# Kernel optimization log

Hardware: AMD Instinct MI355X
Metric: run time of the kernel (lower is better)

The kernel has to match this reference:

```python
import jax, jax.numpy as jnp
import numpy as np

CONF = 0.25      # args.conf
IOU_THR = 0.45   # args.iou
MAX_DET = 300    # args.max_det
NC = 80          # len(model.names)
CAND = 2048      # static cap: top-scoring candidates entering NMS (jit-friendly stand-in for boolean conf mask)


def setup_inputs():
    key = jax.random.key(0)
    pred = jax.random.uniform(key, (16, 4 + NC, 8400), dtype=jnp.float32)
    # first 4 channels are xywh in pixel coordinates for a 640x640 image
    pred = pred.at[:, :4, :].multiply(640.0)
    return {"pred": pred, "img_size": 640}


def xywh2xyxy(b):
    xy, wh = b[..., :2], b[..., 2:4]
    return jnp.concatenate([xy - wh * 0.5, xy + wh * 0.5], axis=-1)


def box_iou(b):
    # b: (K, 4) xyxy -> (K, K) pairwise IoU (torchvision convention)
    x1, y1, x2, y2 = b[:, 0], b[:, 1], b[:, 2], b[:, 3]
    area = (x2 - x1) * (y2 - y1)
    ix1 = jnp.maximum(x1[:, None], x1[None, :])
    iy1 = jnp.maximum(y1[:, None], y1[None, :])
    ix2 = jnp.minimum(x2[:, None], x2[None, :])
    iy2 = jnp.minimum(y2[:, None], y2[None, :])
    inter = jnp.clip(ix2 - ix1, 0.0) * jnp.clip(iy2 - iy1, 0.0)
    return inter / (area[:, None] + area[None, :] - inter + 1e-7)


def nms_keep(nmsbox, valid):
    # Greedy NMS over boxes already sorted by descending score.
    iou = box_iou(nmsbox)  # (CAND, CAND)

    def body(keep, i):
        suppressed = jnp.any(keep & (iou[i] > IOU_THR))
        ki = valid[i] & jnp.logical_not(suppressed)
        return keep.at[i].set(ki), None

    keep0 = jnp.zeros((nmsbox.shape[0],), dtype=bool)
    keep, _ = jax.lax.scan(body, keep0, jnp.arange(nmsbox.shape[0]))
    return keep


def _forward(pred, img_size):
    p = jnp.transpose(pred, (0, 2, 1))           # (N, A, 4+NC)
    boxes_xywh = p[..., :4]
    cls_scores = p[..., 4:4 + NC]
    scores = jnp.max(cls_scores, axis=-1)        # (N, A)
    classes = jnp.argmax(cls_scores, axis=-1)    # (N, A) int

    # static top-CAND candidates (score > conf handled via valid mask below)
    top_s, top_i = jax.lax.top_k(scores, CAND)   # sorted descending
    box = jnp.take_along_axis(boxes_xywh, top_i[..., None], axis=1)  # (N, CAND, 4)
    cls = jnp.take_along_axis(classes, top_i, axis=1)                # (N, CAND)
    box = xywh2xyxy(box)
    inv = 1.0 / img_size                          # multiplier=1, divide by max(H, W)

    def per_image(box_i, score_i, cls_i):
        valid = score_i > CONF
        # class-aware NMS: add class id offset to all 4 normalized coords
        nmsbox = box_i * inv + cls_i[:, None].astype(box_i.dtype)
        keep = nms_keep(nmsbox, valid)
        # kept boxes first, in score order; rest pushed to the end and zeroed
        order = jnp.argsort(jnp.where(keep, jnp.arange(CAND), CAND))[:MAX_DET]
        kept = keep[order].astype(box_i.dtype)[:, None]
        dets = jnp.concatenate(
            [box_i[order], score_i[order, None], cls_i[order, None].astype(box_i.dtype)],
            axis=-1,
        )  # (MAX_DET, 6)
        return dets * kept

    return jax.vmap(per_image)(box, top_s, cls)   # (N, MAX_DET, 6)


def reference(pred, img_size):
    return _forward(pred, img_size)
```

## Files before the change

### kernel.cpp

```cpp
#include <hip/hip_runtime.h>
#include <stdint.h>

#define NB 16
#define NA 8400
#define NA_PAD 9216
#define NCH 84
#define NCLS 80
#define CANDN 2048
#define MAXDET 300

typedef unsigned long long u64;

static const size_t OFF_SU   = 0;
static const size_t OFF_CLS  = 537600;
static const size_t OFF_BOX  = 1075200;
static const size_t OFF_KEY  = 3225600;
static const size_t OFF_NMSB = 3487744;
static const size_t OFF_AREA = 4012032;
static const size_t OFF_H12  = 4143104;
static const size_t OFF_H16  = 4405248;
static const size_t OFF_CLSB = 8599552;

__global__ __launch_bounds__(256) void zero_kernel(int* __restrict__ h) {
  h[blockIdx.x * 256 + threadIdx.x] = 0;
}

__global__ __launch_bounds__(256) void score_kernel(const float* __restrict__ pred,
                                                    unsigned* __restrict__ sug,
                                                    int* __restrict__ cls,
                                                    float4* __restrict__ boxT,
                                                    int* __restrict__ h12,
                                                    int* __restrict__ h16) {
  int a = blockIdx.x * 256 + threadIdx.x;
  int b = blockIdx.y;
  if (a >= NA) return;
  int lane = threadIdx.x & 63;
  const float* pbase = pred + (size_t)b * (NCH * NA);
  const float* p = pbase + 4 * NA + a;
  float best = p[0];
  int bc = 0;
#pragma unroll 8
  for (int c = 1; c < NCLS; ++c) {
    float v = p[(size_t)c * NA];
    if (v > best) { best = v; bc = c; }
  }
  unsigned u = ~__float_as_uint(best);
  sug[(size_t)b * NA + a] = u;
  cls[(size_t)b * NA + a] = bc;
  boxT[(size_t)b * NA + a] =
      make_float4(pbase[a], pbase[NA + a], pbase[2 * NA + a], pbase[3 * NA + a]);
  u64 m = __ballot(true);
  u64 m12 = 0;
#pragma unroll
  for (int bit = 31; bit >= 16; --bit) {
    u64 bb = __ballot((u >> bit) & 1);
    m &= ((u >> bit) & 1) ? bb : ~bb;
    if (bit == 20) m12 = m;
  }
  u64 below = (lane == 0) ? 0ULL : ((1ULL << lane) - 1ULL);
  if ((m12 & below) == 0ULL)
    atomicAdd(&h12[b * 4096 + (int)(u >> 20)], (int)__popcll(m12));
  if ((m & below) == 0ULL)
    atomicAdd(&h16[b * 65536 + (int)(u >> 16)], (int)__popcll(m));
}

__device__ inline u64 shflx64(u64 v, int m) {
  int lo = __shfl_xor((int)(unsigned)(v & 0xFFFFFFFFu), m, 64);
  int hi = __shfl_xor((int)(unsigned)(v >> 32), m, 64);
  return (((u64)(unsigned)hi) << 32) | (unsigned)lo;
}

__device__ inline u64 cswap(u64 a, u64 b, int s, int j, int kk) {
  bool low = (s & j) == 0;
  bool asc = (s & kk) == 0;
  bool takeMin = (low == asc);
  u64 mn = (a < b) ? a : b;
  u64 mx = (a < b) ? b : a;
  return takeMin ? mn : mx;
}

__device__ inline bool iou_gt(float4 bi, float ai, float4 bj, float aj) {
  const double THR = 0x1.CCCCCC8p-2;
  float ix1 = fmaxf(bi.x, bj.x);
  float iy1 = fmaxf(bi.y, bj.y);
  float ix2 = fminf(bi.z, bj.z);
  float iy2 = fminf(bi.w, bj.w);
  float iw = fmaxf(__fsub_rn(ix2, ix1), 0.0f);
  float ih = fmaxf(__fsub_rn(iy2, iy1), 0.0f);
  float inter = __fmul_rn(iw, ih);
  float den = __fadd_rn(__fsub_rn(__fadd_rn(ai, aj), inter), 1e-7f);
  return (double)inter > THR * (double)den;
}

__global__ __launch_bounds__(1024) void select_kernel(const unsigned* __restrict__ sug,
                                                      const int* __restrict__ h12g,
                                                      const int* __restrict__ h16g,
                                                      u64* __restrict__ keybuf) {
  __shared__ alignas(16) unsigned su[NA];
  __shared__ int hist8[256];
  __shared__ int cum[256];
  __shared__ int tielist[1024];
  __shared__ int sl16[16];
  __shared__ int wtot[16];
  __shared__ unsigned sh_pref;
  __shared__ int sh_k, sh_g, sh_cnt;

  int b = blockIdx.x;
  int tid = threadIdx.x;
  int lane = tid & 63;
  int wv = tid >> 6;

  if (tid == 0) { sh_pref = 0; sh_k = CANDN; sh_g = 0; sh_cnt = 0; }

  {
    uint4* su4 = (uint4*)su;
    const uint4* sg4 = (const uint4*)(sug + (size_t)b * NA);
    for (int v = tid; v < NA / 4; v += 1024) su4[v] = sg4[v];
  }

  const int* hb = h12g + b * 4096;
  int4 v = ((const int4*)hb)[tid];
  int ssum = v.x + v.y + v.z + v.w;
  int incl = ssum;
  for (int off = 1; off < 64; off <<= 1) {
    int t = __shfl_up(incl, off, 64);
    if (lane >= off) incl += t;
  }
  if (lane == 63) wtot[wv] = incl;
  __syncthreads();
  if (tid < 16) {
    int w0 = wtot[tid];
    int inc2 = w0;
    for (int off = 1; off < 16; off <<= 1) {
      int t = __shfl_up(inc2, off, 16);
      if (tid >= off) inc2 += t;
    }
    wtot[tid] = inc2 - w0;
  }
  __syncthreads();
  int ebase = wtot[wv] + incl - ssum;
  if (ebase < CANDN && ebase + ssum >= CANDN) {
    int c = ebase;
    int hh[4] = {v.x, v.y, v.z, v.w};
#pragma unroll
    for (int t = 0; t < 4; ++t) {
      if (c + hh[t] >= CANDN) { sh_pref = (unsigned)(tid * 4 + t); sh_k = CANDN - c; break; }
      c += hh[t];
    }
  }
  __syncthreads();
  unsigned B12 = sh_pref;
  int k = sh_k;

  if (tid < 16) sl16[tid] = h16g[(size_t)b * 65536 + B12 * 16 + tid];
  __syncthreads();
  if (tid == 0) {
    int c = 0;
#pragma unroll
    for (int j = 0; j < 16; ++j) {
      int h = sl16[j];
      if (c + h >= k) { sh_pref = (B12 << 4) + (unsigned)j; sh_k = k - c; break; }
      c += h;
    }
  }
  __syncthreads();
  unsigned B16 = sh_pref;
  k = sh_k;

  if (tid < 256) hist8[tid] = 0;
  __syncthreads();
  for (int i = tid; i < NA; i += 1024) {
    unsigned u = su[i];
    if ((u >> 16) == B16) atomicAdd(&hist8[(u >> 8) & 255], 1);
  }
  __syncthreads();
  if (tid < 64) {
    int v0 = hist8[tid * 4 + 0], v1 = hist8[tid * 4 + 1];
    int v2 = hist8[tid * 4 + 2], v3 = hist8[tid * 4 + 3];
    int s0 = v0, s1 = s0 + v1, s2 = s1 + v2, s3 = s2 + v3;
    int tot = s3;
    for (int off = 1; off < 64; off <<= 1) {
      int t = __shfl_up(tot, off, 64);
      if (tid >= off) tot += t;
    }
    int base = tot - s3;
    cum[tid * 4 + 0] = base + s0;
    cum[tid * 4 + 1] = base + s1;
    cum[tid * 4 + 2] = base + s2;
    cum[tid * 4 + 3] = base + s3;
  }
  __syncthreads();
  if (tid < 256) {
    int c = cum[tid];
    int cprev = (tid == 0) ? 0 : cum[tid - 1];
    if (c >= k && cprev < k) {
      sh_pref = (B16 << 16) | ((unsigned)tid << 8);
      sh_k = k - cprev;
    }
  }
  __syncthreads();
  unsigned p24 = sh_pref;
  k = sh_k;

  if (tid < 256) hist8[tid] = 0;
  __syncthreads();
  for (int i = tid; i < NA; i += 1024) {
    unsigned u = su[i];
    if ((u & 0xFFFFFF00u) == p24) atomicAdd(&hist8[u & 255], 1);
  }
  __syncthreads();
  if (tid < 64) {
    int v0 = hist8[tid * 4 + 0], v1 = hist8[tid * 4 + 1];
    int v2 = hist8[tid * 4 + 2], v3 = hist8[tid * 4 + 3];
    int s0 = v0, s1 = s0 + v1, s2 = s1 + v2, s3 = s2 + v3;
    int tot = s3;
    for (int off = 1; off < 64; off <<= 1) {
      int t = __shfl_up(tot, off, 64);
      if (tid >= off) tot += t;
    }
    int base = tot - s3;
    cum[tid * 4 + 0] = base + s0;
    cum[tid * 4 + 1] = base + s1;
    cum[tid * 4 + 2] = base + s2;
    cum[tid * 4 + 3] = base + s3;
  }
  __syncthreads();
  if (tid < 256) {
    int c = cum[tid];
    int cprev = (tid == 0) ? 0 : cum[tid - 1];
    if (c >= k && cprev < k) {
      sh_pref = p24 | (unsigned)tid;
      sh_k = k - cprev;
    }
  }
  __syncthreads();
  unsigned ustar = sh_pref;
  int kp = sh_k;

  for (int i = tid; i < NA; i += 1024) {
    if (su[i] == ustar) {
      int p = atomicAdd(&sh_g, 1);
      if (p < 1024) tielist[p] = i;
    }
  }
  __syncthreads();
  int g = sh_g < 1024 ? sh_g : 1024;

  for (int i = tid; i < NA_PAD; i += 1024) {
    bool act = false;
    u64 key = 0;
    if (i < NA) {
      unsigned u = su[i];
      if (u < ustar) act = true;
      else if (u == ustar) {
        int r = 0;
        for (int t2 = 0; t2 < g; ++t2) r += (tielist[t2] < i);
        act = (r < kp);
      }
      key = (((u64)u) << 32) | (unsigned)i;
    }
    u64 mm = __ballot(act);
    if (mm) {
      int leader = __ffsll(mm) - 1;
      int base = 0;
      if (lane == leader) base = atomicAdd(&sh_cnt, (int)__popcll(mm));
      base = __shfl(base, leader, 64);
      if (act)
        keybuf[(size_t)b * CANDN + base + (int)__popcll(mm & ((1ULL << lane) - 1))] = key;
    }
  }
}

__global__ __launch_bounds__(256) void prep_kernel(const u64* __restrict__ keybuf,
                                                   const int* __restrict__ clsg,
                                                   const float4* __restrict__ boxTg,
                                                   const int* __restrict__ imgsz,
                                                   float4* __restrict__ nmsbG,
                                                   float* __restrict__ areaG,
                                                   unsigned char* __restrict__ clsbG) {
  int s = blockIdx.x * 256 + threadIdx.x;
  int b = blockIdx.y;
  int o = b * CANDN + s;
  u64 key = keybuf[o];
  int idx = (int)(unsigned)(key & 0xFFFFFFFFu);
  float4 bx = boxTg[(size_t)b * NA + idx];
  float inv = (float)(1.0 / (double)imgsz[0]);
  float hw = __fmul_rn(bx.z, 0.5f);
  float hh = __fmul_rn(bx.w, 0.5f);
  float x1 = __fsub_rn(bx.x, hw);
  float y1 = __fsub_rn(bx.y, hh);
  float x2 = __fadd_rn(bx.x, hw);
  float y2 = __fadd_rn(bx.y, hh);
  int ci = clsg[(size_t)b * NA + idx];
  float clsf = (float)ci;
  float nx1 = __fadd_rn(__fmul_rn(x1, inv), clsf);
  float ny1 = __fadd_rn(__fmul_rn(y1, inv), clsf);
  float nx2 = __fadd_rn(__fmul_rn(x2, inv), clsf);
  float ny2 = __fadd_rn(__fmul_rn(y2, inv), clsf);
  float ar = __fmul_rn(__fsub_rn(nx2, nx1), __fsub_rn(ny2, ny1));
  nmsbG[o] = make_float4(nx1, ny1, nx2, ny2);
  areaG[o] = ar;
  clsbG[o] = (unsigned char)ci;
}

__global__ __launch_bounds__(1024) void nms_kernel(const u64* __restrict__ keybuf,
                                                   const float4* __restrict__ nmsbG,
                                                   const float* __restrict__ areaG,
                                                   const unsigned char* __restrict__ clsbG,
                                                   const int* __restrict__ clsg,
                                                   const float4* __restrict__ boxTg,
                                                   float* __restrict__ out) {
  __shared__ alignas(16) u64 skey[CANDN];
  __shared__ alignas(16) float4 nmsb[CANDN];
  __shared__ float areaA[CANDN];
  __shared__ unsigned short a2s[NA];
  __shared__ unsigned char clsA[CANDN];
  __shared__ float4 chunkbox[64];
  __shared__ float chunkarea[64];
  __shared__ float4 bbox[NCLS][16];
  __shared__ float barea[NCLS][16];
  __shared__ int bcount[NCLS];
  __shared__ float4 ovfbox[MAXDET];
  __shared__ float ovfarea[MAXDET];
  __shared__ int idxbuf[MAXDET];
  __shared__ u64 diag[64];
  __shared__ u64 supx[4];
  __shared__ u64 vmaskc;
  __shared__ int sh_nms, sh_ovf;

  int b = blockIdx.x;
  int tid = threadIdx.x;
  int lane = tid & 63;
  int wv = tid >> 6;

  if (tid == 0) { sh_nms = 0; sh_ovf = 0; }
  if (tid < NCLS) bcount[tid] = 0;

  for (int s = tid; s < CANDN; s += 1024) {
    u64 key = keybuf[(size_t)b * CANDN + s];
    skey[s] = key;
    nmsb[s] = nmsbG[(size_t)b * CANDN + s];
    areaA[s] = areaG[(size_t)b * CANDN + s];
    clsA[s] = clsbG[(size_t)b * CANDN + s];
    a2s[(unsigned)(key & 0xFFFFFFFFu)] = (unsigned short)s;
  }
  __syncthreads();

  int s0 = (wv << 7) + lane;
  int s1 = s0 + 64;
  u64 e0 = skey[s0];
  u64 e1 = skey[s1];
  for (int kk = 2; kk <= CANDN; kk <<= 1) {
    for (int j = kk >> 1; j > 0; j >>= 1) {
      if (j >= 128) {
        skey[s0] = e0;
        skey[s1] = e1;
        __syncthreads();
        u64 p0 = skey[s0 ^ j];
        u64 p1 = skey[s1 ^ j];
        e0 = cswap(e0, p0, s0, j, kk);
        e1 = cswap(e1, p1, s1, j, kk);
        __syncthreads();
      } else if (j == 64) {
        bool asc = (s0 & kk) == 0;
        u64 mn = (e0 < e1) ? e0 : e1;
        u64 mx = (e0 < e1) ? e1 : e0;
        e0 = asc ? mn : mx;
        e1 = asc ? mx : mn;
      } else {
        u64 p0 = shflx64(e0, j);
        u64 p1 = shflx64(e1, j);
        e0 = cswap(e0, p0, s0, j, kk);
        e1 = cswap(e1, p1, s1, j, kk);
      }
    }
  }
  skey[s0] = e0;
  skey[s1] = e1;
  __syncthreads();

#pragma unroll 1
  for (int c = 0; c < 32; ++c) {
    __syncthreads();
    int nk0 = sh_nms;
    if (nk0 >= MAXDET) break;
    int rank = (c << 6) + lane;
    u64 mykey = skey[rank];
    int slot = a2s[(unsigned)(mykey & 0xFFFFFFFFu)];
    float4 br = nmsb[slot];
    float arr = areaA[slot];
    int myc = clsA[slot];
    if (wv == 0) {
      chunkbox[lane] = br;
      chunkarea[lane] = arr;
      u64 vb = __ballot(__uint_as_float(~(unsigned)(mykey >> 32)) > 0.25f);
      if (lane == 0) vmaskc = vb;
    }
    if (wv < 3) {
      int cc = myc - 1 + wv;
      bool ok = (cc >= 0 && cc < NCLS);
      int n = ok ? bcount[cc] : 0;
      bool sup = false;
      for (int q = 0; q < n; ++q)
        sup = sup || iou_gt(br, arr, bbox[cc][q], barea[cc][q]);
      u64 sm = __ballot(sup);
      if (lane == 0) supx[wv] = sm;
    } else if (wv == 3) {
      int n = sh_ovf;
      bool sup = false;
      for (int q = 0; q < n; ++q)
        sup = sup || iou_gt(br, arr, ovfbox[q], ovfarea[q]);
      u64 sm = __ballot(sup);
      if (lane == 0) supx[3] = sm;
    }
    __syncthreads();
    u64 tentg = vmaskc & ~(supx[0] | supx[1] | supx[2] | supx[3]);
#pragma unroll
    for (int rr = 0; rr < 4; ++rr) {
      int r = (wv << 2) + rr;
      if ((tentg >> r) & 1ULL) {
        bool supd = iou_gt(chunkbox[r], chunkarea[r], br, arr);
        u64 bb = __ballot(supd);
        if (lane == 0) diag[r] = bb;
      } else if (lane == 0) {
        diag[r] = 0ULL;
      }
    }
    __syncthreads();
    if (wv == 0) {
      bool tent = ((tentg >> lane) & 1ULL) != 0ULL;
      u64 below = (lane == 0) ? 0ULL : ((1ULL << lane) - 1ULL);
      u64 colbelow = diag[lane] & below;
      u64 kept = __ballot(tent);
      for (int it = 0; it < 64; ++it) {
        bool alive = tent && ((kept & colbelow) == 0ULL);
        u64 nk = __ballot(alive);
        if (nk == kept) break;
        kept = nk;
      }
      int cnt = nk0 + (int)__popcll(kept);
      if (cnt > MAXDET) cnt = MAXDET;
      bool mine = ((kept >> lane) & 1ULL) != 0ULL;
      int pos = nk0 + (int)__popcll(kept & below);
      if (mine && pos < MAXDET) {
        idxbuf[pos] = rank;
        int n = atomicAdd(&bcount[myc], 1);
        if (n < 16) { bbox[myc][n] = br; barea[myc][n] = arr; }
        else {
          int mo = atomicAdd(&sh_ovf, 1);
          ovfbox[mo] = br;
          ovfarea[mo] = arr;
        }
      }
      if (lane == 0) sh_nms = cnt;
    }
  }
  __syncthreads();

  int total = sh_nms;
  if (tid < MAXDET) {
    float vals[6] = {0.f, 0.f, 0.f, 0.f, 0.f, 0.f};
    if (tid < total) {
      int rank = idxbuf[tid];
      u64 key = skey[rank];
      int idx = (int)(unsigned)(key & 0xFFFFFFFFu);
      float score = __uint_as_float(~(unsigned)(key >> 32));
      float4 bx = boxTg[(size_t)b * NA + idx];
      float hw = __fmul_rn(bx.z, 0.5f);
      float hh = __fmul_rn(bx.w, 0.5f);
      vals[0] = __fsub_rn(bx.x, hw);
      vals[1] = __fsub_rn(bx.y, hh);
      vals[2] = __fadd_rn(bx.x, hw);
      vals[3] = __fadd_rn(bx.y, hh);
      vals[4] = score;
      vals[5] = (float)clsg[(size_t)b * NA + idx];
    }
#pragma unroll
    for (int q = 0; q < 6; ++q)
      out[((size_t)(b * MAXDET) + tid) * 6 + q] = vals[q];
  }
}

extern "C" void kernel_launch(void* const* d_in, const int* in_sizes, int n_in,
                              void* d_out, int out_size, void* d_ws, size_t ws_size,
                              hipStream_t stream) {
  (void)in_sizes; (void)n_in; (void)out_size; (void)ws_size;
  const float* pred = (const float*)d_in[0];
  const int* imgsz = (const int*)d_in[1];
  char* ws = (char*)d_ws;
  unsigned* sug = (unsigned*)(ws + OFF_SU);
  int* cls = (int*)(ws + OFF_CLS);
  float4* boxT = (float4*)(ws + OFF_BOX);
  u64* keybuf = (u64*)(ws + OFF_KEY);
  float4* nmsbG = (float4*)(ws + OFF_NMSB);
  float* areaG = (float*)(ws + OFF_AREA);
  int* h12 = (int*)(ws + OFF_H12);
  int* h16 = (int*)(ws + OFF_H16);
  unsigned char* clsb = (unsigned char*)(ws + OFF_CLSB);
  float* out = (float*)d_out;

  zero_kernel<<<(262144 + 4194304) / 4 / 256, 256, 0, stream>>>(h12);
  score_kernel<<<dim3((NA + 255) / 256, NB), 256, 0, stream>>>(pred, sug, cls, boxT,
                                                               h12, h16);
  select_kernel<<<NB, 1024, 0, stream>>>(sug, h12, h16, keybuf);
  prep_kernel<<<dim3(CANDN / 256, NB), 256, 0, stream>>>(keybuf, cls, boxT, imgsz,
                                                         nmsbG, areaG, clsb);
  nms_kernel<<<NB, 1024, 0, stream>>>(keybuf, nmsbG, areaG, clsb, cls, boxT, out);
}
```

Before: 66.81 us.

## Run chunked NMS loop in a single wavefront without block barriers

The greedy NMS chunk loop moves from four cooperating wavefronts that hand off through shared memory and several __syncthreads per chunk to a single wavefront that does all the work. That one wave checks the three neighbouring class buckets and the overflow list, then builds the intra-chunk suppression matrix by iterating only over tentatively-kept rows, prefetching the next row. Barrier overhead and the full diagonal pass disappear, but the single wave now does the per-chunk suppression checks serially, with less parallelism.

```diff
diff --git a/kernel.cpp b/kernel.cpp
--- a/kernel.cpp
+++ b/kernel.cpp
@@ -323,9 +323,6 @@
   __shared__ float4 ovfbox[MAXDET];
   __shared__ float ovfarea[MAXDET];
   __shared__ int idxbuf[MAXDET];
-  __shared__ u64 diag[64];
-  __shared__ u64 supx[4];
-  __shared__ u64 vmaskc;
   __shared__ int sh_nms, sh_ovf;
 
   int b = blockIdx.x;
@@ -379,81 +376,92 @@
   skey[s1] = e1;
   __syncthreads();
 
+  if (wv == 0) {
+    int nk0 = 0;
+    int ovf = 0;
+    u64 below = (lane == 0) ? 0ULL : ((1ULL << lane) - 1ULL);
 #pragma unroll 1
-  for (int c = 0; c < 32; ++c) {
-    __syncthreads();
-    int nk0 = sh_nms;
-    if (nk0 >= MAXDET) break;
-    int rank = (c << 6) + lane;
-    u64 mykey = skey[rank];
-    int slot = a2s[(unsigned)(mykey & 0xFFFFFFFFu)];
-    float4 br = nmsb[slot];
-    float arr = areaA[slot];
-    int myc = clsA[slot];
-    if (wv == 0) {
+    for (int c = 0; c < 32 && nk0 < MAXDET; ++c) {
+      int rank = (c << 6) + lane;
+      u64 mykey = skey[rank];
+      int slot = a2s[(unsigned)(mykey & 0xFFFFFFFFu)];
+      float4 br = nmsb[slot];
+      float arr = areaA[slot];
+      int myc = clsA[slot];
       chunkbox[lane] = br;
       chunkarea[lane] = arr;
-      u64 vb = __ballot(__uint_as_float(~(unsigned)(mykey >> 32)) > 0.25f);
-      if (lane == 0) vmaskc = vb;
-    }
-    if (wv < 3) {
-      int cc = myc - 1 + wv;
-      bool ok = (cc >= 0 && cc < NCLS);
-      int n = ok ? bcount[cc] : 0;
+      bool valid = __uint_as_float(~(unsigned)(mykey >> 32)) > 0.25f;
       bool sup = false;
-      for (int q = 0; q < n; ++q)
-        sup = sup || iou_gt(br, arr, bbox[cc][q], barea[cc][q]);
-      u64 sm = __ballot(sup);
-      if (lane == 0) supx[wv] = sm;
-    } else if (wv == 3) {
-      int n = sh_ovf;
-      bool sup = false;
-      for (int q = 0; q < n; ++q)
+#pragma unroll
+      for (int t = 0; t < 3; ++t) {
+        int cc = myc - 1 + t;
+        if (cc >= 0 && cc < NCLS) {
+          int n = bcount[cc];
+          if (n > 16) n = 16;
+          for (int q = 0; q < n; ++q)
+            sup = sup || iou_gt(br, arr, bbox[cc][q], barea[cc][q]);
+        }
+      }
+      for (int q = 0; q < ovf; ++q)
         sup = sup || iou_gt(br, arr, ovfbox[q], ovfarea[q]);
-      u64 sm = __ballot(sup);
-      if (lane == 0) supx[3] = sm;
-    }
-    __syncthreads();
-    u64 tentg = vmaskc & ~(supx[0] | supx[1] | supx[2] | supx[3]);
-#pragma unroll
-    for (int rr = 0; rr < 4; ++rr) {
-      int r = (wv << 2) + rr;
-      if ((tentg >> r) & 1ULL) {
-        bool supd = iou_gt(chunkbox[r], chunkarea[r], br, arr);
-        u64 bb = __ballot(supd);
-        if (lane == 0) diag[r] = bb;
-      } else if (lane == 0) {
-        diag[r] = 0ULL;
+      bool tent = valid && !sup;
+      u64 tentg = __ballot(tent);
+      if (tentg == 0ULL) continue;
+      u64 colb = 0ULL;
+      {
+        u64 mask = tentg;
+        int i0 = -1;
+        float4 b0 = br;
+        float a0 = arr;
+        if (mask) {
+          i0 = __ffsll(mask) - 1;
+          mask &= mask - 1;
+          b0 = chunkbox[i0];
+          a0 = chunkarea[i0];
+        }
+        while (i0 >= 0) {
+          int i1 = -1;
+          float4 b1 = br;
+          float a1 = arr;
+          if (mask) {
+            i1 = __ffsll(mask) - 1;
+            mask &= mask - 1;
+            b1 = chunkbox[i1];
+            a1 = chunkarea[i1];
+          }
+          u64 bb = __ballot(iou_gt(b0, a0, br, arr));
+          if (lane > i0) colb |= ((bb >> lane) & 1ULL) << i0;
+          i0 = i1;
+          b0 = b1;
+          a0 = a1;
+        }
       }
-    }
-    __syncthreads();
-    if (wv == 0) {
-      bool tent = ((tentg >> lane) & 1ULL) != 0ULL;
-      u64 below = (lane == 0) ? 0ULL : ((1ULL << lane) - 1ULL);
-      u64 colbelow = diag[lane] & below;
-      u64 kept = __ballot(tent);
-      for (int it = 0; it < 64; ++it) {
-        bool alive = tent && ((kept & colbelow) == 0ULL);
+      u64 kept = tentg;
+      while (true) {
+        bool alive = tent && ((kept & colb) == 0ULL);
         u64 nk = __ballot(alive);
         if (nk == kept) break;
         kept = nk;
       }
-      int cnt = nk0 + (int)__popcll(kept);
-      if (cnt > MAXDET) cnt = MAXDET;
       bool mine = ((kept >> lane) & 1ULL) != 0ULL;
       int pos = nk0 + (int)__popcll(kept & below);
       if (mine && pos < MAXDET) {
         idxbuf[pos] = rank;
         int n = atomicAdd(&bcount[myc], 1);
-        if (n < 16) { bbox[myc][n] = br; barea[myc][n] = arr; }
-        else {
+        if (n < 16) {
+          bbox[myc][n] = br;
+          barea[myc][n] = arr;
+        } else {
           int mo = atomicAdd(&sh_ovf, 1);
           ovfbox[mo] = br;
           ovfarea[mo] = arr;
         }
       }
-      if (lane == 0) sh_nms = cnt;
-    }
+      nk0 += (int)__popcll(kept);
+      if (nk0 > MAXDET) nk0 = MAXDET;
+      ovf = sh_ovf;
+    }
+    if (lane == 0) sh_nms = nk0;
   }
   __syncthreads();
 
```

Measured after the change: 110.9 us. 1.66x slower.

## Replace in-block bitonic sort with rank-by-counting scatter in prep kernel

Applied to the files above, without the earlier changes.

The per-image bitonic sort of the 2048 candidate keys inside the single-block NMS kernel is replaced by a counting rank in the prep kernel. Each of 128 blocks computes every key's rank by comparing it against all 2048 keys held in shared memory, then scatters the box, area, class and key directly into sorted order. This removes the barrier-heavy sort and the a2s index indirection from the 16-block NMS kernel, spreading the ordering work across many more blocks at the cost of O(N^2) comparisons. The NMS chunk loop also drops one barrier by folding the valid-mask ballot into wave 0 and computing the diagonal IoU for every row unconditionally.

```diff
diff --git a/kernel.cpp b/kernel.cpp
--- a/kernel.cpp
+++ b/kernel.cpp
@@ -20,6 +20,7 @@
 static const size_t OFF_H12  = 4143104;
 static const size_t OFF_H16  = 4405248;
 static const size_t OFF_CLSB = 8599552;
+static const size_t OFF_KEYR = 8632320;
 
 __global__ __launch_bounds__(256) void zero_kernel(int* __restrict__ h) {
   h[blockIdx.x * 256 + threadIdx.x] = 0;
@@ -64,21 +65,6 @@
     atomicAdd(&h16[b * 65536 + (int)(u >> 16)], (int)__popcll(m));
 }
 
-__device__ inline u64 shflx64(u64 v, int m) {
-  int lo = __shfl_xor((int)(unsigned)(v & 0xFFFFFFFFu), m, 64);
-  int hi = __shfl_xor((int)(unsigned)(v >> 32), m, 64);
-  return (((u64)(unsigned)hi) << 32) | (unsigned)lo;
-}
-
-__device__ inline u64 cswap(u64 a, u64 b, int s, int j, int kk) {
-  bool low = (s & j) == 0;
-  bool asc = (s & kk) == 0;
-  bool takeMin = (low == asc);
-  u64 mn = (a < b) ? a : b;
-  u64 mx = (a < b) ? b : a;
-  return takeMin ? mn : mx;
-}
-
 __device__ inline bool iou_gt(float4 bi, float ai, float4 bj, float aj) {
   const double THR = 0x1.CCCCCC8p-2;
   float ix1 = fmaxf(bi.x, bj.x);
@@ -271,18 +257,25 @@
   }
 }
 
-__global__ __launch_bounds__(256) void prep_kernel(const u64* __restrict__ keybuf,
-                                                   const int* __restrict__ clsg,
-                                                   const float4* __restrict__ boxTg,
-                                                   const int* __restrict__ imgsz,
-                                                   float4* __restrict__ nmsbG,
-                                                   float* __restrict__ areaG,
-                                                   unsigned char* __restrict__ clsbG) {
-  int s = blockIdx.x * 256 + threadIdx.x;
+__global__ __launch_bounds__(256) void rankprep_kernel(const u64* __restrict__ keybuf,
+                                                       const int* __restrict__ clsg,
+                                                       const float4* __restrict__ boxTg,
+                                                       const int* __restrict__ imgsz,
+                                                       u64* __restrict__ skeyR,
+                                                       float4* __restrict__ nmsbR,
+                                                       float* __restrict__ areaR,
+                                                       unsigned char* __restrict__ clsR) {
+  __shared__ alignas(16) u64 kb[CANDN];
   int b = blockIdx.y;
-  int o = b * CANDN + s;
-  u64 key = keybuf[o];
-  int idx = (int)(unsigned)(key & 0xFFFFFFFFu);
+  int tid = threadIdx.x;
+  for (int i = tid; i < CANDN; i += 256) kb[i] = keybuf[(size_t)b * CANDN + i];
+  __syncthreads();
+  int s = blockIdx.x * 256 + tid;
+  u64 mykey = kb[s];
+  int rank = 0;
+#pragma unroll 16
+  for (int j = 0; j < CANDN; ++j) rank += (kb[j] < mykey);
+  int idx = (int)(unsigned)(mykey & 0xFFFFFFFFu);
   float4 bx = boxTg[(size_t)b * NA + idx];
   float inv = (float)(1.0 / (double)imgsz[0]);
   float hw = __fmul_rn(bx.z, 0.5f);
@@ -298,12 +291,14 @@
   float nx2 = __fadd_rn(__fmul_rn(x2, inv), clsf);
   float ny2 = __fadd_rn(__fmul_rn(y2, inv), clsf);
   float ar = __fmul_rn(__fsub_rn(nx2, nx1), __fsub_rn(ny2, ny1));
-  nmsbG[o] = make_float4(nx1, ny1, nx2, ny2);
-  areaG[o] = ar;
-  clsbG[o] = (unsigned char)ci;
-}
-
-__global__ __launch_bounds__(1024) void nms_kernel(const u64* __restrict__ keybuf,
+  int o = b * CANDN + rank;
+  skeyR[o] = mykey;
+  nmsbR[o] = make_float4(nx1, ny1, nx2, ny2);
+  areaR[o] = ar;
+  clsR[o] = (unsigned char)ci;
+}
+
+__global__ __launch_bounds__(1024) void nms_kernel(const u64* __restrict__ skeyRg,
                                                    const float4* __restrict__ nmsbG,
                                                    const float* __restrict__ areaG,
                                                    const unsigned char* __restrict__ clsbG,
@@ -313,10 +308,7 @@
   __shared__ alignas(16) u64 skey[CANDN];
   __shared__ alignas(16) float4 nmsb[CANDN];
   __shared__ float areaA[CANDN];
-  __shared__ unsigned short a2s[NA];
   __shared__ unsigned char clsA[CANDN];
-  __shared__ float4 chunkbox[64];
-  __shared__ float chunkarea[64];
   __shared__ float4 bbox[NCLS][16];
   __shared__ float barea[NCLS][16];
   __shared__ int bcount[NCLS];
@@ -325,7 +317,6 @@
   __shared__ int idxbuf[MAXDET];
   __shared__ u64 diag[64];
   __shared__ u64 supx[4];
-  __shared__ u64 vmaskc;
   __shared__ int sh_nms, sh_ovf;
 
   int b = blockIdx.x;
@@ -337,47 +328,11 @@
   if (tid < NCLS) bcount[tid] = 0;
 
   for (int s = tid; s < CANDN; s += 1024) {
-    u64 key = keybuf[(size_t)b * CANDN + s];
-    skey[s] = key;
+    skey[s] = skeyRg[(size_t)b * CANDN + s];
     nmsb[s] = nmsbG[(size_t)b * CANDN + s];
     areaA[s] = areaG[(size_t)b * CANDN + s];
     clsA[s] = clsbG[(size_t)b * CANDN + s];
-    a2s[(unsigned)(key & 0xFFFFFFFFu)] = (unsigned short)s;
-  }
-  __syncthreads();
-
-  int s0 = (wv << 7) + lane;
-  int s1 = s0 + 64;
-  u64 e0 = skey[s0];
-  u64 e1 = skey[s1];
-  for (int kk = 2; kk <= CANDN; kk <<= 1) {
-    for (int j = kk >> 1; j > 0; j >>= 1) {
-      if (j >= 128) {
-        skey[s0] = e0;
-        skey[s1] = e1;
-        __syncthreads();
-        u64 p0 = skey[s0 ^ j];
-        u64 p1 = skey[s1 ^ j];
-        e0 = cswap(e0, p0, s0, j, kk);
-        e1 = cswap(e1, p1, s1, j, kk);
-        __syncthreads();
-      } else if (j == 64) {
-        bool asc = (s0 & kk) == 0;
-        u64 mn = (e0 < e1) ? e0 : e1;
-        u64 mx = (e0 < e1) ? e1 : e0;
-        e0 = asc ? mn : mx;
-        e1 = asc ? mx : mn;
-      } else {
-        u64 p0 = shflx64(e0, j);
-        u64 p1 = shflx64(e1, j);
-        e0 = cswap(e0, p0, s0, j, kk);
-        e1 = cswap(e1, p1, s1, j, kk);
-      }
-    }
-  }
-  skey[s0] = e0;
-  skey[s1] = e1;
-  __syncthreads();
+  }
 
 #pragma unroll 1
   for (int c = 0; c < 32; ++c) {
@@ -385,21 +340,14 @@
     int nk0 = sh_nms;
     if (nk0 >= MAXDET) break;
     int rank = (c << 6) + lane;
-    u64 mykey = skey[rank];
-    int slot = a2s[(unsigned)(mykey & 0xFFFFFFFFu)];
-    float4 br = nmsb[slot];
-    float arr = areaA[slot];
-    int myc = clsA[slot];
-    if (wv == 0) {
-      chunkbox[lane] = br;
-      chunkarea[lane] = arr;
-      u64 vb = __ballot(__uint_as_float(~(unsigned)(mykey >> 32)) > 0.25f);
-      if (lane == 0) vmaskc = vb;
-    }
+    float4 br = nmsb[rank];
+    float arr = areaA[rank];
+    int myc = clsA[rank];
     if (wv < 3) {
       int cc = myc - 1 + wv;
       bool ok = (cc >= 0 && cc < NCLS);
       int n = ok ? bcount[cc] : 0;
+      if (n > 16) n = 16;
       bool sup = false;
       for (int q = 0; q < n; ++q)
         sup = sup || iou_gt(br, arr, bbox[cc][q], barea[cc][q]);
@@ -413,27 +361,25 @@
       u64 sm = __ballot(sup);
       if (lane == 0) supx[3] = sm;
     }
-    __syncthreads();
-    u64 tentg = vmaskc & ~(supx[0] | supx[1] | supx[2] | supx[3]);
 #pragma unroll
     for (int rr = 0; rr < 4; ++rr) {
       int r = (wv << 2) + rr;
-      if ((tentg >> r) & 1ULL) {
-        bool supd = iou_gt(chunkbox[r], chunkarea[r], br, arr);
-        u64 bb = __ballot(supd);
-        if (lane == 0) diag[r] = bb;
-      } else if (lane == 0) {
-        diag[r] = 0ULL;
-      }
+      bool supd = iou_gt(nmsb[(c << 6) + r], areaA[(c << 6) + r], br, arr);
+      u64 bb = __ballot(supd);
+      if (lane == 0) diag[r] = bb;
     }
     __syncthreads();
     if (wv == 0) {
+      bool valid = __uint_as_float(~(unsigned)(skey[rank] >> 32)) > 0.25f;
+      u64 vb = __ballot(valid);
+      u64 orsup = supx[0] | supx[1] | supx[2] | supx[3];
+      u64 tentg = vb & ~orsup;
       bool tent = ((tentg >> lane) & 1ULL) != 0ULL;
       u64 below = (lane == 0) ? 0ULL : ((1ULL << lane) - 1ULL);
-      u64 colbelow = diag[lane] & below;
-      u64 kept = __ballot(tent);
-      for (int it = 0; it < 64; ++it) {
-        bool alive = tent && ((kept & colbelow) == 0ULL);
+      u64 colb = diag[lane] & below;
+      u64 kept = tentg;
+      while (true) {
+        bool alive = tent && ((kept & colb) == 0ULL);
         u64 nk = __ballot(alive);
         if (nk == kept) break;
         kept = nk;
@@ -445,8 +391,10 @@
       if (mine && pos < MAXDET) {
         idxbuf[pos] = rank;
         int n = atomicAdd(&bcount[myc], 1);
-        if (n < 16) { bbox[myc][n] = br; barea[myc][n] = arr; }
-        else {
+        if (n < 16) {
+          bbox[myc][n] = br;
+          barea[myc][n] = arr;
+        } else {
           int mo = atomicAdd(&sh_ovf, 1);
           ovfbox[mo] = br;
           ovfarea[mo] = arr;
@@ -492,18 +440,19 @@
   int* cls = (int*)(ws + OFF_CLS);
   float4* boxT = (float4*)(ws + OFF_BOX);
   u64* keybuf = (u64*)(ws + OFF_KEY);
-  float4* nmsbG = (float4*)(ws + OFF_NMSB);
-  float* areaG = (float*)(ws + OFF_AREA);
+  float4* nmsbR = (float4*)(ws + OFF_NMSB);
+  float* areaR = (float*)(ws + OFF_AREA);
   int* h12 = (int*)(ws + OFF_H12);
   int* h16 = (int*)(ws + OFF_H16);
-  unsigned char* clsb = (unsigned char*)(ws + OFF_CLSB);
+  unsigned char* clsR = (unsigned char*)(ws + OFF_CLSB);
+  u64* skeyR = (u64*)(ws + OFF_KEYR);
   float* out = (float*)d_out;
 
   zero_kernel<<<(262144 + 4194304) / 4 / 256, 256, 0, stream>>>(h12);
   score_kernel<<<dim3((NA + 255) / 256, NB), 256, 0, stream>>>(pred, sug, cls, boxT,
                                                                h12, h16);
   select_kernel<<<NB, 1024, 0, stream>>>(sug, h12, h16, keybuf);
-  prep_kernel<<<dim3(CANDN / 256, NB), 256, 0, stream>>>(keybuf, cls, boxT, imgsz,
-                                                         nmsbG, areaG, clsb);
-  nms_kernel<<<NB, 1024, 0, stream>>>(keybuf, nmsbG, areaG, clsb, cls, boxT, out);
-}
+  rankprep_kernel<<<dim3(CANDN / 256, NB), 256, 0, stream>>>(keybuf, cls, boxT, imgsz,
+                                                             skeyR, nmsbR, areaR, clsR);
+  nms_kernel<<<NB, 1024, 0, stream>>>(skeyR, nmsbR, areaR, clsR, cls, boxT, out);
+}
```

Result: slower. 69.45 us (+4.0%).
